# Optimization experiments

Hardware: AMD Instinct MI355X
Metric: run time of the kernel (lower is better)

Reference implementation:

```python
import jax, jax.numpy as jnp
import numpy as np

B, N, K, D_MODEL = 4, 16384, 32, 64

def gather_neighbors(x, idx):
    # x: [B, N, F], idx: [B, N, K] -> [B, N, K, F]
    return jnp.take_along_axis(x[:, :, None, :], idx[:, :, :, None], axis=1)

def setup_inputs() -> dict:
    key = jax.random.key(0)
    k1, k2, k3, k4, k5 = jax.random.split(key, 5)
    x = jax.random.normal(k1, (B, N, D_MODEL), dtype=jnp.float32)
    pos = jax.random.normal(k2, (B, N, 3), dtype=jnp.float32)
    neighbor_idx = jax.random.randint(k3, (B, N, K), 0, N, dtype=jnp.int32)
    W1 = jax.random.normal(k4, (3, D_MODEL), dtype=jnp.float32) * (1.0 / np.sqrt(3.0))
    b1 = jnp.zeros((D_MODEL,), dtype=jnp.float32)
    W2 = jax.random.normal(k5, (D_MODEL, D_MODEL), dtype=jnp.float32) * (1.0 / np.sqrt(D_MODEL))
    b2 = jnp.zeros((D_MODEL,), dtype=jnp.float32)
    return {"x": x, "pos": pos, "neighbor_idx": neighbor_idx,
            "W1": W1, "b1": b1, "W2": W2, "b2": b2}

def reference(x, pos, neighbor_idx, W1, b1, W2, b2):
    # gather neighbor positions: [B, N, K, 3]
    neighbors = gather_neighbors(pos, neighbor_idx)
    rel_pos = pos[:, :, None, :] - neighbors              # [B, N, K, 3]
    # weight MLP: Linear(3,d) + LeakyReLU(0.1), Linear(d,d)
    h = jax.nn.leaky_relu(jnp.einsum('bnkd,df->bnkf', rel_pos, W1) + b1, 0.1)
    w = jnp.einsum('bnkf,fg->bnkg', h, W2) + b2           # [B, N, K, F]
    xg = gather_neighbors(x, neighbor_idx)                # [B, N, K, F]
    return jnp.sum(w * xg, axis=2)                        # [B, N, F]
```

## Files before the change

kernel.cpp:

```cpp
#include <hip/hip_runtime.h>


#define NPTS   16384
#define KNB    32
#define F      64
#define BATCH  4
#define LOG2N  14
#define WPTS   4

typedef short    bf16x8 __attribute__((ext_vector_type(8)));
typedef float    f32x16 __attribute__((ext_vector_type(16)));
typedef _Float16 half4  __attribute__((ext_vector_type(4)));

static __device__ __forceinline__ unsigned rne_hi(float f) {
    unsigned u = __builtin_bit_cast(unsigned, f);
    return u + 0x7FFFu + ((u >> 16) & 1u);
}
static __device__ __forceinline__ int pack2_bf16(float lo, float hi) {
    return (int)__builtin_amdgcn_perm(rne_hi(hi), rne_hi(lo), 0x07060302u);
}

__global__ __launch_bounds__(256, 2) void pointconv_mfma(
    const float* __restrict__ x,
    const float* __restrict__ pos,
    const int*   __restrict__ idx,
    const float* __restrict__ W1,
    const float* __restrict__ b1,
    const float* __restrict__ W2,
    const float* __restrict__ b2,
    float*       __restrict__ out)
{
    __shared__ __align__(16) half4 w1lds[F];
    __shared__ __align__(16) short w2lds[F][72];

    const int tid = threadIdx.x;
    if (tid < F) {
        w1lds[tid] = (half4){ (_Float16)W1[0 * F + tid], (_Float16)W1[1 * F + tid],
                              (_Float16)W1[2 * F + tid], (_Float16)b1[tid] };
    }
#pragma unroll
    for (int r = 0; r < 16; ++r) {
        const int e = r * 256 + tid;
        const int g = e >> 6, f = e & 63;
        w2lds[f][g] = (short)(rne_hi(W2[e]) >> 16);
    }
    __syncthreads();

    const int lane = tid & 63;
    const int wv   = tid >> 6;
    const int m    = lane & 31;
    const int half = lane >> 5;

    bf16x8 bfrag[4][2];
#pragma unroll
    for (int t = 0; t < 4; ++t)
#pragma unroll
        for (int c = 0; c < 2; ++c)
            bfrag[t][c] = *(const bf16x8*)&w2lds[32 * c + m][16 * t + 8 * half];

    const float b20 = b2[m];
    const float b21 = b2[32 + m];

    const int p0   = (blockIdx.x * 4 + wv) * WPTS;
    const int base = (p0 >> LOG2N) << LOG2N;

    int jm[WPTS];
#pragma unroll
    for (int i = 0; i < WPTS; ++i) jm[i] = idx[(p0 + i) * KNB + m];

    float rx[WPTS], ry[WPTS], rz[WPTS];
#pragma unroll
    for (int i = 0; i < WPTS; ++i) {
        const int p = p0 + i;
        const float px = pos[p * 3 + 0];
        const float py = pos[p * 3 + 1];
        const float pz = pos[p * 3 + 2];
        const int nr = base + jm[i];
        rx[i] = px - pos[nr * 3 + 0];
        ry[i] = py - pos[nr * 3 + 1];
        rz[i] = pz - pos[nr * 3 + 2];
    }

#pragma unroll
    for (int i = 0; i < WPTS; ++i) {
        const int p = p0 + i;

        float xa[16], xb[16];
#pragma unroll
        for (int reg = 0; reg < 16; ++reg) {
            const int row = (reg & 3) + ((reg >> 2) << 3) + (half << 2);
            const int jk  = __shfl(jm[i], row);
            const float* xr = x + (size_t)(base + jk) * F;
            xa[reg] = xr[m];
            xb[reg] = xr[32 + m];
        }

        f32x16 acc0, acc1;
#pragma unroll
        for (int r = 0; r < 16; ++r) { acc0[r] = 0.f; acc1[r] = 0.f; }

#pragma unroll
        for (int t = 0; t < 4; ++t) {
            int hpk[4];
#pragma unroll
            for (int jj = 0; jj < 4; ++jj) {
                float hv[2];
#pragma unroll
                for (int s = 0; s < 2; ++s) {
                    const int g = 16 * t + 8 * half + 2 * jj + s;
                    const half4 w = w1lds[g];
                    float a = (float)w[3];
                    a = fmaf(rx[i], (float)w[0], a);
                    a = fmaf(ry[i], (float)w[1], a);
                    a = fmaf(rz[i], (float)w[2], a);
                    hv[s] = fmaxf(a, 0.1f * a);
                }
                hpk[jj] = pack2_bf16(hv[0], hv[1]);
            }
            const bf16x8 af = __builtin_bit_cast(bf16x8, *(int4*)hpk);
            acc0 = __builtin_amdgcn_mfma_f32_32x32x16_bf16(af, bfrag[t][0], acc0, 0, 0, 0);
            acc1 = __builtin_amdgcn_mfma_f32_32x32x16_bf16(af, bfrag[t][1], acc1, 0, 0, 0);
        }

        float s0a = 0.f, s0b = 0.f, s1a = 0.f, s1b = 0.f;
#pragma unroll
        for (int reg = 0; reg < 16; reg += 2) {
            s0a = fmaf(acc0[reg]     + b20, xa[reg],     s0a);
            s0b = fmaf(acc0[reg + 1] + b20, xa[reg + 1], s0b);
            s1a = fmaf(acc1[reg]     + b21, xb[reg],     s1a);
            s1b = fmaf(acc1[reg + 1] + b21, xb[reg + 1], s1b);
        }
        float s0 = s0a + s0b, s1 = s1a + s1b;
        s0 += __shfl_xor(s0, 32);
        s1 += __shfl_xor(s1, 32);
        out[p * F + half * 32 + m] = half ? s1 : s0;
    }
}

extern "C" void kernel_launch(void* const* d_in, const int* in_sizes, int n_in,
                              void* d_out, int out_size, void* d_ws, size_t ws_size,
                              hipStream_t stream) {
    const float* x   = (const float*)d_in[0];
    const float* pos = (const float*)d_in[1];
    const int*   idx = (const int*)  d_in[2];
    const float* W1  = (const float*)d_in[3];
    const float* b1  = (const float*)d_in[4];
    const float* W2  = (const float*)d_in[5];
    const float* b2  = (const float*)d_in[6];
    float* out = (float*)d_out;

    dim3 grid((BATCH * NPTS) / (4 * WPTS));
    dim3 block(256);
    pointconv_mfma<<<grid, block, 0, stream>>>(x, pos, idx, W1, b1, W2, b2, out);
}
```

Before: 163.6 us.

## Switch to fp16 packed MLP and f16 MFMA, float2 gathers, scalar index loads

Replaces the bf16 path with fp16. The first layer is now evaluated with packed half2 FMAs and the MFMA uses the f16 variant, which removes the manual bf16 rounding and packing. W2 columns are interleaved so each lane handles the adjacent features 2m and 2m+1, which allows float2 gathers of x and float2 output stores. Neighbor indices come from wave-uniform scalar loads instead of lane shuffles, b2 is folded into the accumulator initialisation, and the occupancy hint rises to 4 blocks per CU. The trade-off is that computing the hidden layer in fp16 reduces precision, and the higher occupancy target may force register spills.

Result: slower. 343.5 us (+110.0%).

```diff
diff --git a/kernel.cpp b/kernel.cpp
--- a/kernel.cpp
+++ b/kernel.cpp
@@ -8,19 +8,11 @@
 #define LOG2N  14
 #define WPTS   4
 
-typedef short    bf16x8 __attribute__((ext_vector_type(8)));
+typedef _Float16 h2     __attribute__((ext_vector_type(2)));
+typedef _Float16 h8     __attribute__((ext_vector_type(8)));
 typedef float    f32x16 __attribute__((ext_vector_type(16)));
-typedef _Float16 half4  __attribute__((ext_vector_type(4)));
 
-static __device__ __forceinline__ unsigned rne_hi(float f) {
-    unsigned u = __builtin_bit_cast(unsigned, f);
-    return u + 0x7FFFu + ((u >> 16) & 1u);
-}
-static __device__ __forceinline__ int pack2_bf16(float lo, float hi) {
-    return (int)__builtin_amdgcn_perm(rne_hi(hi), rne_hi(lo), 0x07060302u);
-}
-
-__global__ __launch_bounds__(256, 2) void pointconv_mfma(
+__global__ __launch_bounds__(256, 4) void pointconv_mfma(
     const float* __restrict__ x,
     const float* __restrict__ pos,
     const int*   __restrict__ idx,
@@ -30,39 +22,41 @@
     const float* __restrict__ b2,
     float*       __restrict__ out)
 {
-    __shared__ __align__(16) half4 w1lds[F];
-    __shared__ __align__(16) short w2lds[F][72];
+    __shared__ __align__(16) _Float16 w1p[32][8];
+    __shared__ __align__(16) _Float16 w2h[F][72];
 
     const int tid = threadIdx.x;
-    if (tid < F) {
-        w1lds[tid] = (half4){ (_Float16)W1[0 * F + tid], (_Float16)W1[1 * F + tid],
-                              (_Float16)W1[2 * F + tid], (_Float16)b1[tid] };
+    if (tid < 32) {
+        const int g = 2 * tid;
+        w1p[tid][0] = (_Float16)W1[0 * F + g]; w1p[tid][1] = (_Float16)W1[0 * F + g + 1];
+        w1p[tid][2] = (_Float16)W1[1 * F + g]; w1p[tid][3] = (_Float16)W1[1 * F + g + 1];
+        w1p[tid][4] = (_Float16)W1[2 * F + g]; w1p[tid][5] = (_Float16)W1[2 * F + g + 1];
+        w1p[tid][6] = (_Float16)b1[g];         w1p[tid][7] = (_Float16)b1[g + 1];
     }
 #pragma unroll
     for (int r = 0; r < 16; ++r) {
         const int e = r * 256 + tid;
-        const int g = e >> 6, f = e & 63;
-        w2lds[f][g] = (short)(rne_hi(W2[e]) >> 16);
+        w2h[e & 63][e >> 6] = (_Float16)W2[e];
     }
     __syncthreads();
 
     const int lane = tid & 63;
     const int wv   = tid >> 6;
     const int m    = lane & 31;
-    const int half = lane >> 5;
+    const int hf   = lane >> 5;
 
-    bf16x8 bfrag[4][2];
+    h8 bfrag[4][2];
 #pragma unroll
     for (int t = 0; t < 4; ++t)
 #pragma unroll
         for (int c = 0; c < 2; ++c)
-            bfrag[t][c] = *(const bf16x8*)&w2lds[32 * c + m][16 * t + 8 * half];
+            bfrag[t][c] = *(const h8*)&w2h[2 * m + c][16 * t + 8 * hf];
 
-    const float b20 = b2[m];
-    const float b21 = b2[32 + m];
+    const float2 b2v = *(const float2*)(b2 + 2 * m);
 
     const int p0   = (blockIdx.x * 4 + wv) * WPTS;
     const int base = (p0 >> LOG2N) << LOG2N;
+    const float* __restrict__ xb2 = x + (size_t)base * F + 2 * m;
 
     int jm[WPTS];
 #pragma unroll
@@ -81,59 +75,65 @@
         rz[i] = pz - pos[nr * 3 + 2];
     }
 
+    const h2 c01 = { (_Float16)0.1f, (_Float16)0.1f };
+
 #pragma unroll
     for (int i = 0; i < WPTS; ++i) {
-        const int p = p0 + i;
+        const int p   = p0 + i;
+        const int p_s = __builtin_amdgcn_readfirstlane(p);
+        const int* __restrict__ rowp = idx + (size_t)p_s * KNB;
+        int js[KNB];
+#pragma unroll
+        for (int c = 0; c < KNB; ++c) js[c] = rowp[c];
 
-        float xa[16], xb[16];
+        float2 xv[16];
 #pragma unroll
         for (int reg = 0; reg < 16; ++reg) {
-            const int row = (reg & 3) + ((reg >> 2) << 3) + (half << 2);
-            const int jk  = __shfl(jm[i], row);
-            const float* xr = x + (size_t)(base + jk) * F;
-            xa[reg] = xr[m];
-            xb[reg] = xr[32 + m];
+            const int rA = (reg & 3) + ((reg >> 2) << 3);
+            const int jk = hf ? js[rA + 4] : js[rA];
+            xv[reg] = *(const float2*)(xb2 + (size_t)jk * F);
         }
 
         f32x16 acc0, acc1;
 #pragma unroll
-        for (int r = 0; r < 16; ++r) { acc0[r] = 0.f; acc1[r] = 0.f; }
+        for (int r = 0; r < 16; ++r) { acc0[r] = b2v.x; acc1[r] = b2v.y; }
+
+        h2 rxp = { (_Float16)rx[i], (_Float16)rx[i] };
+        h2 ryp = { (_Float16)ry[i], (_Float16)ry[i] };
+        h2 rzp = { (_Float16)rz[i], (_Float16)rz[i] };
 
 #pragma unroll
         for (int t = 0; t < 4; ++t) {
-            int hpk[4];
+            h8 af;
 #pragma unroll
             for (int jj = 0; jj < 4; ++jj) {
-                float hv[2];
-#pragma unroll
-                for (int s = 0; s < 2; ++s) {
-                    const int g = 16 * t + 8 * half + 2 * jj + s;
-                    const half4 w = w1lds[g];
-                    float a = (float)w[3];
-                    a = fmaf(rx[i], (float)w[0], a);
-                    a = fmaf(ry[i], (float)w[1], a);
-                    a = fmaf(rz[i], (float)w[2], a);
-                    hv[s] = fmaxf(a, 0.1f * a);
-                }
-                hpk[jj] = pack2_bf16(hv[0], hv[1]);
+                const int g2 = 8 * t + 4 * hf + jj;
+                const h8 w = *(const h8*)&w1p[g2][0];
+                const h2 wx = __builtin_shufflevector(w, w, 0, 1);
+                const h2 wy = __builtin_shufflevector(w, w, 2, 3);
+                const h2 wz = __builtin_shufflevector(w, w, 4, 5);
+                const h2 bb = __builtin_shufflevector(w, w, 6, 7);
+                h2 hv = bb + rxp * wx;
+                hv = hv + ryp * wy;
+                hv = hv + rzp * wz;
+                hv = __builtin_elementwise_max(hv, hv * c01);
+                af[2 * jj]     = hv[0];
+                af[2 * jj + 1] = hv[1];
             }
-            const bf16x8 af = __builtin_bit_cast(bf16x8, *(int4*)hpk);
-            acc0 = __builtin_amdgcn_mfma_f32_32x32x16_bf16(af, bfrag[t][0], acc0, 0, 0, 0);
-            acc1 = __builtin_amdgcn_mfma_f32_32x32x16_bf16(af, bfrag[t][1], acc1, 0, 0, 0);
+            acc0 = __builtin_amdgcn_mfma_f32_32x32x16_f16(af, bfrag[t][0], acc0, 0, 0, 0);
+            acc1 = __builtin_amdgcn_mfma_f32_32x32x16_f16(af, bfrag[t][1], acc1, 0, 0, 0);
         }
 
-        float s0a = 0.f, s0b = 0.f, s1a = 0.f, s1b = 0.f;
+        float s0 = 0.f, s1 = 0.f;
 #pragma unroll
-        for (int reg = 0; reg < 16; reg += 2) {
-            s0a = fmaf(acc0[reg]     + b20, xa[reg],     s0a);
-            s0b = fmaf(acc0[reg + 1] + b20, xa[reg + 1], s0b);
-            s1a = fmaf(acc1[reg]     + b21, xb[reg],     s1a);
-            s1b = fmaf(acc1[reg + 1] + b21, xb[reg + 1], s1b);
+        for (int reg = 0; reg < 16; ++reg) {
+            s0 = fmaf(acc0[reg], xv[reg].x, s0);
+            s1 = fmaf(acc1[reg], xv[reg].y, s1);
         }
-        float s0 = s0a + s0b, s1 = s1a + s1b;
         s0 += __shfl_xor(s0, 32);
         s1 += __shfl_xor(s1, 32);
-        out[p * F + half * 32 + m] = half ? s1 : s0;
+        if (hf == 0)
+            *(float2*)(out + (size_t)p * F + 2 * m) = make_float2(s0, s1);
     }
 }
 
```
